# Performance work log

Hardware: AMD Instinct MI355X
Metric: run time of the kernel (lower is better)

## Reference

```python
import jax, jax.numpy as jnp
import numpy as np

B, L, LF = 4096, 200, 100
E, P, H = 64, 32, 32      # embed_dim, prompt_embed_dim, prompt_net_hidden_size
IV, UV = 100000, 50000    # item/user vocab
IFD, UFD = 128, 128       # item/user raw feature dims
PNET = E * H + H + H * P + P  # per-sample MLP param count


def _forward(item_emb, user_emb, W_if, b_if, W_uf, b_uf, Wp, bp,
             Wf1, bf1, Wf2, bf2, Wf3, item_features, user_features,
             user_id, target_item_id, history_item_id, history_len,
             item_pos_feedback, item_pos_feedback_mask,
             item_neg_feedback, item_neg_feedback_mask):
    # ---- backbone embeddings ----
    tgt = item_emb[target_item_id]              # [B,E]
    hist = item_emb[history_item_id]            # [B,L,E]
    item_feat_e = jax.nn.sigmoid(item_features @ W_if + b_if)   # [B,E]
    user_feat_e = jax.nn.sigmoid(user_features @ W_uf + b_uf)   # [B,E]
    # attention sequence pooling over history (length-masked softmax)
    valid = jnp.arange(L)[None, :] < history_len[:, None]        # [B,L]
    scores = jnp.einsum('be,ble->bl', tgt, hist) / jnp.sqrt(jnp.float32(E))
    scores = jnp.where(valid, scores, jnp.float32(-1e9))
    attn = jax.nn.softmax(scores, axis=-1)
    hist_pooled = jnp.einsum('bl,ble->be', attn, hist)           # [B,E]
    final_user_embed = user_emb[user_id] + user_feat_e + hist_pooled  # [B,E]
    final_item_embed = tgt + item_feat_e                              # [B,E]

    # ---- prompt input: masked mean over positive feedback ----
    pos_fb = item_emb[item_pos_feedback]        # [B,LF,E]
    pm = item_pos_feedback_mask.astype(jnp.float32)   # [B,LF,1]
    prompt_input = (pos_fb * pm).sum(axis=1) / pm.sum(axis=1)   # [B,E]

    # ---- hypernetwork: generate per-sample MLP weights ----
    total_prompt = jax.nn.relu(prompt_input @ Wp + bp)  # [B, P+PNET]
    prompt_embed = total_prompt[:, :P]
    pnet = total_prompt[:, P:]
    s1 = E * H
    w1 = pnet[:, :s1].reshape(-1, E, H)                 # [B,E,H]
    b1 = pnet[:, s1:s1 + H]                             # [B,H]
    w2 = pnet[:, s1 + H:s1 + H + H * P].reshape(-1, H, P)  # [B,H,P]
    b2 = pnet[:, s1 + H + H * P:]                       # [B,P]

    def prompt_mlp(u):  # u: [B,Lf,E] -> [B,Lf,P]
        h = jax.nn.relu(jnp.einsum('ble,beh->blh', u, w1) + b1[:, None, :])
        return jnp.einsum('blh,bhp->blp', h, w2) + b2[:, None, :]

    pos_pe = jnp.where(item_pos_feedback_mask, prompt_mlp(pos_fb), 0.0).sum(axis=1)  # [B,P]
    neg_fb = item_emb[item_neg_feedback]
    neg_pe = jnp.where(item_neg_feedback_mask, prompt_mlp(neg_fb), 0.0).sum(axis=1)  # [B,P]
    loss_pfpe = jax.nn.softplus(-(pos_pe - neg_pe))     # [B,P]

    # ---- fusion + dot-product scoring ----
    fusion_in = jnp.concatenate([final_item_embed, pos_pe, prompt_embed], axis=1)  # [B,E+2P]
    h = jax.nn.relu(fusion_in @ Wf1 + bf1)
    h = jax.nn.relu(h @ Wf2 + bf2)
    fused_item = h @ Wf3                                # [B,E], last layer: no bias/act
    output = jnp.sum(final_user_embed * fused_item, axis=1, keepdims=True)  # [B,1]
    return output, loss_pfpe


def setup_inputs() -> dict:
    key = jax.random.key(0)
    ks = jax.random.split(key, 20)
    g = lambda i, shape, s=0.05: jax.random.normal(ks[i], shape, jnp.float32) * s
    pm = jax.random.randint(ks[14], (B, LF, 1), 0, 2).astype(bool).at[:, 0, :].set(True)
    nm = jax.random.randint(ks[15], (B, LF, 1), 0, 2).astype(bool).at[:, 0, :].set(True)
    return {
        'item_emb': g(0, (IV, E)),
        'user_emb': g(1, (UV, E)),
        'W_if': g(2, (IFD, E)), 'b_if': jnp.zeros((E,), jnp.float32),
        'W_uf': g(3, (UFD, E)), 'b_uf': jnp.zeros((E,), jnp.float32),
        'Wp': g(4, (E, P + PNET)), 'bp': jnp.zeros((P + PNET,), jnp.float32),
        'Wf1': g(5, (E + 2 * P, 200)), 'bf1': jnp.zeros((200,), jnp.float32),
        'Wf2': g(6, (200, 80)), 'bf2': jnp.zeros((80,), jnp.float32),
        'Wf3': g(7, (80, E)),
        'item_features': jax.random.normal(ks[8], (B, IFD), jnp.float32),
        'user_features': jax.random.normal(ks[9], (B, UFD), jnp.float32),
        'user_id': jax.random.randint(ks[10], (B,), 0, UV),
        'target_item_id': jax.random.randint(ks[11], (B,), 0, IV),
        'history_item_id': jax.random.randint(ks[12], (B, L), 0, IV),
        'history_len': jax.random.randint(ks[13], (B,), 1, L + 1),
        'item_pos_feedback': jax.random.randint(ks[16], (B, LF), 0, IV),
        'item_pos_feedback_mask': pm,
        'item_neg_feedback': jax.random.randint(ks[17], (B, LF), 0, IV),
        'item_neg_feedback_mask': nm,
    }


def reference(item_emb, user_emb, W_if, b_if, W_uf, b_uf, Wp, bp,
              Wf1, bf1, Wf2, bf2, Wf3, item_features, user_features,
              user_id, target_item_id, history_item_id, history_len,
              item_pos_feedback, item_pos_feedback_mask,
              item_neg_feedback, item_neg_feedback_mask):
    return _forward(item_emb, user_emb, W_if, b_if, W_uf, b_uf, Wp, bp,
                    Wf1, bf1, Wf2, bf2, Wf3, item_features, user_features,
                    user_id, target_item_id, history_item_id, history_len,
                    item_pos_feedback, item_pos_feedback_mask,
                    item_neg_feedback, item_neg_feedback_mask)
```

## Files before the change

kernel.cpp:

```cpp
#include <hip/hip_runtime.h>
#include <hip/hip_bf16.h>
#include <hip/hip_fp16.h>
#include <math.h>

#define BN 4096
#define LH 200
#define LFB 100
#define ED 64
#define PD 32
#define HD 32
#define NP 3168
#define IV 100000

typedef unsigned int uint32;
typedef __attribute__((ext_vector_type(8))) short short8;
typedef __attribute__((ext_vector_type(8))) _Float16 half8;
typedef __attribute__((ext_vector_type(4))) float f32x4;
union BF8 { uint32 u[4]; short8 v; };
union HF8 { uint32 u[4]; half8 v; };

__device__ __forceinline__ uint32 f2bf_pack(float x, float y) {
    uint32 ux = __float_as_uint(x);
    uint32 uy = __float_as_uint(y);
    uint32 bx = (ux + 0x7fffu + ((ux >> 16) & 1u)) >> 16;
    uint32 by = (uy + 0x7fffu + ((uy >> 16) & 1u)) >> 16;
    return (by << 16) | (bx & 0xffffu);
}

__device__ __forceinline__ uint32 f2h_pack(float x, float y) {
    __half2 h = __floats2half2_rn(x, y);
    return *(reinterpret_cast<uint32*>(&h));
}

__global__ __launch_bounds__(256) void k0_cvt(
    const float* __restrict__ src, uint32* __restrict__ dst)
{
    const int i = blockIdx.x * 256 + threadIdx.x;
    const float2 v = ((const float2*)src)[i];
    dst[i] = f2bf_pack(v.x, v.y);
}

__global__ __launch_bounds__(256) void k0b_cvt_wp(
    const float* __restrict__ Wp, uint32* __restrict__ WpB)
{
    const int n = blockIdx.x * 256 + threadIdx.x;
    const int kw = blockIdx.y;
    if (n < NP) {
        const float a = Wp[(size_t)(2*kw)*NP + n];
        const float b = Wp[(size_t)(2*kw+1)*NP + n];
        WpB[(size_t)n*32 + kw] = f2bf_pack(a, b);
    }
}

__global__ __launch_bounds__(256) void k0c_cvt_wf(
    const float* __restrict__ Wf1, const float* __restrict__ Wf2,
    const float* __restrict__ Wf3, uint32* __restrict__ W1B,
    uint32* __restrict__ W2B, uint32* __restrict__ W3B)
{
    const int i = blockIdx.x * 256 + threadIdx.x;
    if (i < 13312) {
        const int n = i >> 6, kw = i & 63;
        W1B[i] = (n < 200) ? f2h_pack(Wf1[(size_t)(2*kw)*200 + n],
                                      Wf1[(size_t)(2*kw+1)*200 + n]) : 0u;
    } else if (i < 22272) {
        const int j = i - 13312, n = j / 112, kw = j % 112;
        W2B[j] = (kw < 100) ? f2h_pack(Wf2[(size_t)(2*kw)*80 + n],
                                       Wf2[(size_t)(2*kw+1)*80 + n]) : 0u;
    } else if (i < 25344) {
        const int j = i - 22272, n = j / 48, kw = j % 48;
        W3B[j] = (kw < 40) ? f2h_pack(Wf3[(size_t)(2*kw)*64 + n],
                                      Wf3[(size_t)(2*kw+1)*64 + n]) : 0u;
    }
}

#define HS 33
__global__ __launch_bounds__(256, 4) void k1_gather_attn(
    const uint32* __restrict__ IEB,
    const float* __restrict__ item_emb, const float* __restrict__ user_emb,
    const float* __restrict__ W_if, const float* __restrict__ b_if,
    const float* __restrict__ W_uf, const float* __restrict__ b_uf,
    const float* __restrict__ item_features, const float* __restrict__ user_features,
    const int* __restrict__ user_id, const int* __restrict__ target_item_id,
    const int* __restrict__ hist_id, const int* __restrict__ hist_len,
    const int* __restrict__ pos_fb, const int* __restrict__ pos_mask,
    float* __restrict__ FUE, float* __restrict__ FIE, uint32* __restrict__ PINB)
{
    const int b = blockIdx.x;
    const int t = threadIdx.x;
    const int w = t >> 6;
    const int lane = t & 63;

    __shared__ __align__(16) float tgt[64];
    __shared__ float feats[256];
    __shared__ float ufe[64];
    __shared__ float scoreS[256];
    __shared__ float wred[8];
    __shared__ float part[256];
    __shared__ float part2[256];
    __shared__ float cntw[4];
    __shared__ int   hids[200];
    __shared__ uint32 hist2[200*HS];

    const int hl = hist_len[b];
    if (t < 200) hids[t] = hist_id[(size_t)b*LH + t];
    feats[t] = (t < 128) ? item_features[(size_t)b*128 + t]
                         : user_features[(size_t)b*128 + (t-128)];
    if (t < 64) tgt[t] = item_emb[(size_t)target_item_id[b]*64 + t];
    __syncthreads();

    const int kk = lane & 31;
    const int hf = lane >> 5;
    #pragma unroll
    for (int i = 0; i < 25; i++) {
        const int l = w*50 + i*2 + hf;
        hist2[l*HS + kk] = IEB[(size_t)hids[l]*32 + kk];
    }

    {
        const int wk = lane >> 1;
        const int comp = lane & 1;
        float acc = 0.f, cnt = 0.f;
        const int l0 = w * 25;
        const int* pid = pos_fb + (size_t)b*LFB;
        const int* pmk = pos_mask + (size_t)b*LFB;
        for (int g = 0; g < 5; g++) {
            const int base = l0 + g*5;
            int m0 = pmk[base+0], m1 = pmk[base+1], m2 = pmk[base+2],
                m3 = pmk[base+3], m4 = pmk[base+4];
            int i0 = pid[base+0], i1 = pid[base+1], i2 = pid[base+2],
                i3 = pid[base+3], i4 = pid[base+4];
            uint32 w0 = IEB[(size_t)i0*32 + wk];
            uint32 w1 = IEB[(size_t)i1*32 + wk];
            uint32 w2 = IEB[(size_t)i2*32 + wk];
            uint32 w3 = IEB[(size_t)i3*32 + wk];
            uint32 w4 = IEB[(size_t)i4*32 + wk];
            float v0 = __uint_as_float(comp ? (w0 & 0xffff0000u) : (w0 << 16));
            float v1 = __uint_as_float(comp ? (w1 & 0xffff0000u) : (w1 << 16));
            float v2 = __uint_as_float(comp ? (w2 & 0xffff0000u) : (w2 << 16));
            float v3 = __uint_as_float(comp ? (w3 & 0xffff0000u) : (w3 << 16));
            float v4 = __uint_as_float(comp ? (w4 & 0xffff0000u) : (w4 << 16));
            float f0 = m0 ? 1.f : 0.f, f1 = m1 ? 1.f : 0.f, f2 = m2 ? 1.f : 0.f,
                  f3 = m3 ? 1.f : 0.f, f4 = m4 ? 1.f : 0.f;
            acc = fmaf(f0, v0, acc); acc = fmaf(f1, v1, acc);
            acc = fmaf(f2, v2, acc); acc = fmaf(f3, v3, acc);
            acc = fmaf(f4, v4, acc);
            cnt += f0 + f1 + f2 + f3 + f4;
        }
        part2[w*64 + lane] = acc;
        if (lane == 0) cntw[w] = cnt;
    }

    if (w == 0) {
        float acc = b_if[lane];
        #pragma unroll 4
        for (int k = 0; k < 128; k++) acc = fmaf(feats[k], W_if[k*64 + lane], acc);
        FIE[(size_t)b*64 + lane] = tgt[lane] + 1.f / (1.f + __expf(-acc));
    } else if (w == 1) {
        float acc = b_uf[lane];
        #pragma unroll 4
        for (int k = 0; k < 128; k++) acc = fmaf(feats[128 + k], W_uf[k*64 + lane], acc);
        ufe[lane] = 1.f / (1.f + __expf(-acc));
    }
    __syncthreads();

    float sc = -1e9f;
    if (t < 200) {
        const uint32* hrow = &hist2[t*HS];
        float acc = 0.f;
        #pragma unroll 8
        for (int k2 = 0; k2 < 32; k2++) {
            const uint32 word = hrow[k2];
            const float2 tf = ((const float2*)tgt)[k2];
            acc = fmaf(__uint_as_float(word << 16),        tf.x, acc);
            acc = fmaf(__uint_as_float(word & 0xffff0000u), tf.y, acc);
        }
        if (t < hl) sc = acc * 0.125f;
    }

    float m = sc;
    #pragma unroll
    for (int off = 32; off >= 1; off >>= 1) m = fmaxf(m, __shfl_xor(m, off, 64));
    if (lane == 0) wred[w] = m;
    __syncthreads();
    const float mx = fmaxf(fmaxf(wred[0], wred[1]), fmaxf(wred[2], wred[3]));
    const float ev = __expf(sc - mx);
    float s = ev;
    #pragma unroll
    for (int off = 32; off >= 1; off >>= 1) s += __shfl_xor(s, off, 64);
    if (lane == 0) wred[4 + w] = s;
    __syncthreads();
    const float S = wred[4] + wred[5] + wred[6] + wred[7];
    if (t < 200) scoreS[t] = ev / S;
    __syncthreads();

    {
        const int comp = lane & 1;
        const int wk = lane >> 1;
        float acc = 0.f;
        #pragma unroll 5
        for (int l = w*50; l < w*50 + 50; l++) {
            const uint32 word = hist2[l*HS + wk];
            const float hv = __uint_as_float(comp ? (word & 0xffff0000u) : (word << 16));
            acc = fmaf(scoreS[l], hv, acc);
        }
        part[w*64 + lane] = acc;
    }
    __syncthreads();

    if (t < 64) {
        const float c = cntw[0] + cntw[1] + cntw[2] + cntw[3];
        const float pooled = part[t] + part[64+t] + part[128+t] + part[192+t];
        const float pinv = (part2[t] + part2[64+t] + part2[128+t] + part2[192+t]) / c;
        FUE[(size_t)b*64 + t] = user_emb[(size_t)user_id[b]*64 + t] + ufe[t] + pooled;
        const float po = __shfl_xor(pinv, 1, 64);
        if ((t & 1) == 0) PINB[(size_t)b*32 + (t >> 1)] = f2bf_pack(pinv, po);
    }
}

__global__ __launch_bounds__(256) void k2_prompt_gemm(
    const uint32* __restrict__ PINB, const uint32* __restrict__ WpB,
    const float* __restrict__ bp, float* __restrict__ TP32,
    uint32* __restrict__ TPN)
{
    __shared__ uint32 As[64*36];
    __shared__ uint32 Bs[128*36];
    __shared__ float bps[128];
    const int t = threadIdx.x;
    const int m0 = blockIdx.y * 64;
    const int n0 = blockIdx.x * 128;

    {
        const int m = t >> 2, kw0 = (t & 3) * 8;
        const uint4 u0 = *(const uint4*)&PINB[(size_t)(m0+m)*32 + kw0];
        const uint4 u1 = *(const uint4*)&PINB[(size_t)(m0+m)*32 + kw0 + 4];
        *(uint4*)&As[m*36 + kw0]     = u0;
        *(uint4*)&As[m*36 + kw0 + 4] = u1;
    }
    {
        const int n = t >> 1, kw0 = (t & 1) * 16;
        const int gn = n0 + n;
        if (gn < NP) {
            #pragma unroll
            for (int j = 0; j < 4; j++) {
                const uint4 u = *(const uint4*)&WpB[(size_t)gn*32 + kw0 + 4*j];
                *(uint4*)&Bs[n*36 + kw0 + 4*j] = u;
            }
        } else {
            #pragma unroll
            for (int j = 0; j < 16; j++) Bs[n*36 + kw0 + j] = 0u;
        }
    }
    if (t < 128) bps[t] = (n0 + t < NP) ? bp[n0 + t] : 0.f;
    __syncthreads();

    const int w = t >> 6, lane = t & 63, ml = lane & 15, q = lane >> 4;

    BF8 a0, a1;
    { uint4 u = *(const uint4*)&As[(w*16+ml)*36 + q*4];      a0.u[0]=u.x; a0.u[1]=u.y; a0.u[2]=u.z; a0.u[3]=u.w; }
    { uint4 u = *(const uint4*)&As[(w*16+ml)*36 + 16 + q*4]; a1.u[0]=u.x; a1.u[1]=u.y; a1.u[2]=u.z; a1.u[3]=u.w; }

    f32x4 c[8];
    #pragma unroll
    for (int nb = 0; nb < 8; nb++) {
        BF8 b0, b1;
        { uint4 u = *(const uint4*)&Bs[(nb*16+ml)*36 + q*4];      b0.u[0]=u.x; b0.u[1]=u.y; b0.u[2]=u.z; b0.u[3]=u.w; }
        { uint4 u = *(const uint4*)&Bs[(nb*16+ml)*36 + 16 + q*4]; b1.u[0]=u.x; b1.u[1]=u.y; b1.u[2]=u.z; b1.u[3]=u.w; }
        f32x4 cc = {0.f, 0.f, 0.f, 0.f};
        cc = __builtin_amdgcn_mfma_f32_16x16x32_bf16(a0.v, b0.v, cc, 0, 0, 0);
        cc = __builtin_amdgcn_mfma_f32_16x16x32_bf16(a1.v, b1.v, cc, 0, 0, 0);
        c[nb] = cc;
    }

    #pragma unroll
    for (int nb = 0; nb < 8; nb++) {
        const int n = n0 + nb*16 + ml;
        const float bv = bps[nb*16 + ml];
        #pragma unroll
        for (int r = 0; r < 4; r++) {
            const int m = m0 + w*16 + q*4 + r;
            const float v = fmaxf(c[nb][r] + bv, 0.f);
            const float vp = __shfl_xor(v, 1, 64);
            if (n < 32) {
                TP32[(size_t)m*32 + n] = v;
            } else if (n < NP && (ml & 1) == 0) {
                TPN[(size_t)m*1568 + ((n - 32) >> 1)] = f2bf_pack(v, vp);
            }
        }
    }
}

__global__ __launch_bounds__(256) void k3_prompt_mlp(
    const uint32* __restrict__ IEB,
    const int* __restrict__ pos_fb, const int* __restrict__ pos_mask,
    const int* __restrict__ neg_fb, const int* __restrict__ neg_mask,
    const uint32* __restrict__ TPN,
    float* __restrict__ POS_PE, float* __restrict__ out)
{
    const int b = blockIdx.x, t = threadIdx.x;
    const int w = t >> 6, lane = t & 63;
    const int ml = lane & 15, q = lane >> 4;

    __shared__ uint32 w1b[32*36];
    __shared__ uint32 w2b[32*20];
    __shared__ float b1s[32], b2s[32];
    __shared__ float mP[208], mN[208];
    __shared__ int ids[208];
    __shared__ float Hs[4][16*36];
    __shared__ float wps[4][4][16];

    const uint32* pnw = TPN + (size_t)b*1568;
    #pragma unroll
    for (int it = 0; it < 4; it++) {
        const int i = t + 256*it;
        const int n = i >> 5, kw = i & 31;
        const uint32 wa = pnw[kw*32 + (n >> 1)];
        const uint32 wb = pnw[kw*32 + 16 + (n >> 1)];
        const uint32 h0 = (n & 1) ? (wa >> 16) : (wa & 0xffffu);
        const uint32 h1 = (n & 1) ? (wb >> 16) : (wb & 0xffffu);
        w1b[n*36 + kw] = h0 | (h1 << 16);
    }
    #pragma unroll
    for (int it = 0; it < 2; it++) {
        const int i = t + 256*it;
        const int n = i >> 4, kw = i & 15;
        const uint32 wa = pnw[1040 + kw*32 + (n >> 1)];
        const uint32 wb = pnw[1040 + kw*32 + 16 + (n >> 1)];
        const uint32 h0 = (n & 1) ? (wa >> 16) : (wa & 0xffffu);
        const uint32 h1 = (n & 1) ? (wb >> 16) : (wb & 0xffffu);
        w2b[n*20 + kw] = h0 | (h1 << 16);
    }
    if (t < 16) {
        const uint32 wa = pnw[1024 + t];
        b1s[2*t]   = __uint_as_float(wa << 16);
        b1s[2*t+1] = __uint_as_float(wa & 0xffff0000u);
        const uint32 wb = pnw[1552 + t];
        b2s[2*t]   = __uint_as_float(wb << 16);
        b2s[2*t+1] = __uint_as_float(wb & 0xffff0000u);
    }
    if (t < 208) {
        int id = 0; float p = 0.f, nn = 0.f;
        if (t < 100) {
            id = pos_fb[(size_t)b*LFB + t];
            p  = (pos_mask[(size_t)b*LFB + t] != 0) ? 1.f : 0.f;
        } else if (t < 200) {
            const int li = t - 100;
            id = neg_fb[(size_t)b*LFB + li];
            nn = (neg_mask[(size_t)b*LFB + li] != 0) ? 1.f : 0.f;
        }
        ids[t] = id; mP[t] = p; mN[t] = nn;
    }
    __syncthreads();

    BF8 bf100, bf110, bf101, bf111, bf20, bf21;
    {
        uint4 u;
        u = *(const uint4*)&w1b[ml*36 + q*4];            bf100.u[0]=u.x; bf100.u[1]=u.y; bf100.u[2]=u.z; bf100.u[3]=u.w;
        u = *(const uint4*)&w1b[ml*36 + 16 + q*4];       bf110.u[0]=u.x; bf110.u[1]=u.y; bf110.u[2]=u.z; bf110.u[3]=u.w;
        u = *(const uint4*)&w1b[(16+ml)*36 + q*4];       bf101.u[0]=u.x; bf101.u[1]=u.y; bf101.u[2]=u.z; bf101.u[3]=u.w;
        u = *(const uint4*)&w1b[(16+ml)*36 + 16 + q*4];  bf111.u[0]=u.x; bf111.u[1]=u.y; bf111.u[2]=u.z; bf111.u[3]=u.w;
        u = *(const uint4*)&w2b[ml*20 + q*4];            bf20.u[0]=u.x;  bf20.u[1]=u.y;  bf20.u[2]=u.z;  bf20.u[3]=u.w;
        u = *(const uint4*)&w2b[(16+ml)*20 + q*4];       bf21.u[0]=u.x;  bf21.u[1]=u.y;  bf21.u[2]=u.z;  bf21.u[3]=u.w;
    }

    float accP0=0.f, accP1=0.f, accN0=0.f, accN1=0.f;
    float* hsw = Hs[w];

    for (int tile = w; tile < 13; tile += 4) {
        const int g = tile*16 + ml;
        const uint32* rowp = IEB + (size_t)ids[g]*32;
        BF8 a0, a1;
        { uint4 u = *(const uint4*)(rowp + q*4);      a0.u[0]=u.x; a0.u[1]=u.y; a0.u[2]=u.z; a0.u[3]=u.w; }
        { uint4 u = *(const uint4*)(rowp + 16 + q*4); a1.u[0]=u.x; a1.u[1]=u.y; a1.u[2]=u.z; a1.u[3]=u.w; }

        f32x4 c0 = {0.f,0.f,0.f,0.f}, c1 = {0.f,0.f,0.f,0.f};
        c0 = __builtin_amdgcn_mfma_f32_16x16x32_bf16(a0.v, bf100.v, c0, 0, 0, 0);
        c0 = __builtin_amdgcn_mfma_f32_16x16x32_bf16(a1.v, bf110.v, c0, 0, 0, 0);
        c1 = __builtin_amdgcn_mfma_f32_16x16x32_bf16(a0.v, bf101.v, c1, 0, 0, 0);
        c1 = __builtin_amdgcn_mfma_f32_16x16x32_bf16(a1.v, bf111.v, c1, 0, 0, 0);

        #pragma unroll
        for (int r = 0; r < 4; r++) {
            const int row = q*4 + r;
            hsw[row*36 + ml]      = fmaxf(c0[r] + b1s[ml],      0.f);
            hsw[row*36 + 16 + ml] = fmaxf(c1[r] + b1s[16 + ml], 0.f);
        }
        asm volatile("s_waitcnt lgkmcnt(0)" ::: "memory");

        const float4 h0 = *(const float4*)&hsw[ml*36 + q*8];
        const float4 h1 = *(const float4*)&hsw[ml*36 + q*8 + 4];
        BF8 a2;
        a2.u[0] = f2bf_pack(h0.x, h0.y);
        a2.u[1] = f2bf_pack(h0.z, h0.w);
        a2.u[2] = f2bf_pack(h1.x, h1.y);
        a2.u[3] = f2bf_pack(h1.z, h1.w);

        f32x4 d0 = {0.f,0.f,0.f,0.f}, d1 = {0.f,0.f,0.f,0.f};
        d0 = __builtin_amdgcn_mfma_f32_16x16x32_bf16(a2.v, bf20.v, d0, 0, 0, 0);
        d1 = __builtin_amdgcn_mfma_f32_16x16x32_bf16(a2.v, bf21.v, d1, 0, 0, 0);

        #pragma unroll
        for (int r = 0; r < 4; r++) {
            const int g2 = tile*16 + q*4 + r;
            const float o0 = d0[r] + b2s[ml];
            const float o1 = d1[r] + b2s[16 + ml];
            accP0 = fmaf(mP[g2], o0, accP0);
            accP1 = fmaf(mP[g2], o1, accP1);
            accN0 = fmaf(mN[g2], o0, accN0);
            accN1 = fmaf(mN[g2], o1, accN1);
        }
    }

    accP0 += __shfl_xor(accP0, 16, 64); accP0 += __shfl_xor(accP0, 32, 64);
    accP1 += __shfl_xor(accP1, 16, 64); accP1 += __shfl_xor(accP1, 32, 64);
    accN0 += __shfl_xor(accN0, 16, 64); accN0 += __shfl_xor(accN0, 32, 64);
    accN1 += __shfl_xor(accN1, 16, 64); accN1 += __shfl_xor(accN1, 32, 64);
    if (lane < 16) {
        wps[w][0][lane] = accP0;
        wps[w][1][lane] = accP1;
        wps[w][2][lane] = accN0;
        wps[w][3][lane] = accN1;
    }
    __syncthreads();

    if (t < 32) {
        const int nt = t >> 4, p = t & 15;
        const float pp = wps[0][nt][p] + wps[1][nt][p] + wps[2][nt][p] + wps[3][nt][p];
        const float nn = wps[0][2+nt][p] + wps[1][2+nt][p] + wps[2][2+nt][p] + wps[3][2+nt][p];
        POS_PE[(size_t)b*32 + t] = pp;
        const float x = nn - pp;
        out[BN + (size_t)b*32 + t] = fmaxf(x, 0.f) + log1pf(__expf(-fabsf(x)));
    }
}

__global__ __launch_bounds__(256) void k4_fusion(
    const float* __restrict__ FUE, const float* __restrict__ FIE,
    const float* __restrict__ POS_PE, const float* __restrict__ TP32,
    const uint32* __restrict__ W1B, const uint32* __restrict__ W2B,
    const uint32* __restrict__ W3B,
    const float* __restrict__ bf1, const float* __restrict__ bf2,
    float* __restrict__ out)
{
    const int b0 = blockIdx.x * 16;
    const int t = threadIdx.x;
    const int w = t >> 6, lane = t & 63, ml = lane & 15, q = lane >> 4;

    __shared__ uint32 w1s[208*68];
    __shared__ uint32 w2s[80*116];
    __shared__ uint32 w3s[64*52];
    __shared__ uint32 fin[16*68];
    __shared__ uint32 h1w[16*116];
    __shared__ uint32 h2w[16*52];
    __shared__ float fuels[16*68];
    __shared__ float b1s[208], b2s[80];
    __shared__ float part4[4][16];

    for (int i = t; i < 13312; i += 256) w1s[(i >> 6)*68 + (i & 63)] = W1B[i];
    for (int i = t; i < 8960; i += 256)  w2s[(i / 112)*116 + (i % 112)] = W2B[i];
    for (int i = t; i < 3072; i += 256)  w3s[(i / 48)*52 + (i % 48)] = W3B[i];

    #pragma unroll
    for (int it = 0; it < 4; it++) {
        const int i = t + 256*it;
        const int m2 = i >> 6, kw = i & 63;
        const int row = b0 + m2;
        float a, c;
        if (kw < 32)      { const float2 v = *(const float2*)&FIE[(size_t)row*64 + 2*kw];          a = v.x; c = v.y; }
        else if (kw < 48) { const float2 v = *(const float2*)&POS_PE[(size_t)row*32 + 2*kw - 64];  a = v.x; c = v.y; }
        else              { const float2 v = *(const float2*)&TP32[(size_t)row*32 + 2*kw - 96];    a = v.x; c = v.y; }
        fin[m2*68 + kw] = f2h_pack(a, c);
        fuels[m2*68 + kw] = FUE[(size_t)row*64 + kw];
    }
    if (t < 208) b1s[t] = (t < 200) ? bf1[t] : 0.f;
    if (t < 80)  b2s[t] = bf2[t];
    if (t < 128) {
        h1w[(t >> 3)*116 + 104 + (t & 7)] = 0u;
        h2w[(t >> 3)*52 + 40 + (t & 7)] = 0u;
    }
    __syncthreads();

    HF8 a1f[4];
    #pragma unroll
    for (int s = 0; s < 4; s++) {
        const uint4 u = *(const uint4*)&fin[ml*68 + s*16 + q*4];
        a1f[s].u[0] = u.x; a1f[s].u[1] = u.y; a1f[s].u[2] = u.z; a1f[s].u[3] = u.w;
    }
    for (int nt = w; nt < 13; nt += 4) {
        const uint32* wrow = &w1s[(16*nt + ml)*68];
        f32x4 c = {0.f, 0.f, 0.f, 0.f};
        #pragma unroll
        for (int s = 0; s < 4; s++) {
            HF8 bfm;
            const uint4 u = *(const uint4*)&wrow[s*16 + q*4];
            bfm.u[0] = u.x; bfm.u[1] = u.y; bfm.u[2] = u.z; bfm.u[3] = u.w;
            c = __builtin_amdgcn_mfma_f32_16x16x32_f16(a1f[s].v, bfm.v, c, 0, 0, 0);
        }
        const float bv = b1s[16*nt + ml];
        #pragma unroll
        for (int r = 0; r < 4; r++) {
            const float v = fmaxf(c[r] + bv, 0.f);
            const float vp = __shfl_xor(v, 1, 64);
            if ((ml & 1) == 0)
                h1w[(q*4 + r)*116 + 8*nt + (ml >> 1)] = f2h_pack(v, vp);
        }
    }
    __syncthreads();

    HF8 a2f[7];
    #pragma unroll
    for (int s = 0; s < 7; s++) {
        const uint4 u = *(const uint4*)&h1w[ml*116 + s*16 + q*4];
        a2f[s].u[0] = u.x; a2f[s].u[1] = u.y; a2f[s].u[2] = u.z; a2f[s].u[3] = u.w;
    }
    for (int nt = w; nt < 5; nt += 4) {
        const uint32* wrow = &w2s[(16*nt + ml)*116];
        f32x4 c = {0.f, 0.f, 0.f, 0.f};
        #pragma unroll
        for (int s = 0; s < 7; s++) {
            HF8 bfm;
            const uint4 u = *(const uint4*)&wrow[s*16 + q*4];
            bfm.u[0] = u.x; bfm.u[1] = u.y; bfm.u[2] = u.z; bfm.u[3] = u.w;
            c = __builtin_amdgcn_mfma_f32_16x16x32_f16(a2f[s].v, bfm.v, c, 0, 0, 0);
        }
        const float bv = b2s[16*nt + ml];
        #pragma unroll
        for (int r = 0; r < 4; r++) {
            const float v = fmaxf(c[r] + bv, 0.f);
            const float vp = __shfl_xor(v, 1, 64);
            if ((ml & 1) == 0)
                h2w[(q*4 + r)*52 + 8*nt + (ml >> 1)] = f2h_pack(v, vp);
        }
    }
    __syncthreads();

    {
        const int nt = w;
        const uint32* wrow = &w3s[(16*nt + ml)*52];
        f32x4 c = {0.f, 0.f, 0.f, 0.f};
        #pragma unroll
        for (int s = 0; s < 3; s++) {
            HF8 afm, bfm;
            const uint4 ua = *(const uint4*)&h2w[ml*52 + s*16 + q*4];
            afm.u[0] = ua.x; afm.u[1] = ua.y; afm.u[2] = ua.z; afm.u[3] = ua.w;
            const uint4 ub = *(const uint4*)&wrow[s*16 + q*4];
            bfm.u[0] = ub.x; bfm.u[1] = ub.y; bfm.u[2] = ub.z; bfm.u[3] = ub.w;
            c = __builtin_amdgcn_mfma_f32_16x16x32_f16(afm.v, bfm.v, c, 0, 0, 0);
        }
        #pragma unroll
        for (int r = 0; r < 4; r++) {
            float p = c[r] * fuels[(q*4 + r)*68 + 16*nt + ml];
            p += __shfl_xor(p, 1, 64);
            p += __shfl_xor(p, 2, 64);
            p += __shfl_xor(p, 4, 64);
            p += __shfl_xor(p, 8, 64);
            if (ml == 0) part4[w][q*4 + r] = p;
        }
    }
    __syncthreads();

    if (t < 16) out[b0 + t] = part4[0][t] + part4[1][t] + part4[2][t] + part4[3][t];
}

extern "C" void kernel_launch(void* const* d_in, const int* in_sizes, int n_in,
                              void* d_out, int out_size, void* d_ws, size_t ws_size,
                              hipStream_t stream)
{
    const float* item_emb       = (const float*)d_in[0];
    const float* user_emb       = (const float*)d_in[1];
    const float* W_if           = (const float*)d_in[2];
    const float* b_if           = (const float*)d_in[3];
    const float* W_uf           = (const float*)d_in[4];
    const float* b_uf           = (const float*)d_in[5];
    const float* Wp             = (const float*)d_in[6];
    const float* bp             = (const float*)d_in[7];
    const float* Wf1            = (const float*)d_in[8];
    const float* bf1            = (const float*)d_in[9];
    const float* Wf2            = (const float*)d_in[10];
    const float* bf2            = (const float*)d_in[11];
    const float* Wf3            = (const float*)d_in[12];
    const float* item_features  = (const float*)d_in[13];
    const float* user_features  = (const float*)d_in[14];
    const int*   user_id        = (const int*)d_in[15];
    const int*   target_item_id = (const int*)d_in[16];
    const int*   history_item_id= (const int*)d_in[17];
    const int*   history_len    = (const int*)d_in[18];
    const int*   pos_fb         = (const int*)d_in[19];
    const int*   pos_mask       = (const int*)d_in[20];
    const int*   neg_fb         = (const int*)d_in[21];
    const int*   neg_mask       = (const int*)d_in[22];

    float* out = (float*)d_out;
    float* ws  = (float*)d_ws;

    uint32* IEB  = (uint32*)ws;
    uint32* WpB  = IEB + (size_t)IV*32;
    uint32* W1B  = WpB + (size_t)NP*32;
    uint32* W2B  = W1B + 13312;
    uint32* W3B  = W2B + 8960;
    uint32* PINB = W3B + 3072;
    float*  FUE  = (float*)(PINB + (size_t)BN*32);
    float*  FIE  = FUE + (size_t)BN*64;
    float*  TP32 = FIE + (size_t)BN*64;
    uint32* TPN  = (uint32*)(TP32 + (size_t)BN*32);
    float*  PPE  = (float*)(TPN + (size_t)BN*1568);

    k0_cvt<<<dim3(IV*32/256), dim3(256), 0, stream>>>(item_emb, IEB);
    k0b_cvt_wp<<<dim3(13, 32), dim3(256), 0, stream>>>(Wp, WpB);
    k0c_cvt_wf<<<dim3(99), dim3(256), 0, stream>>>(Wf1, Wf2, Wf3, W1B, W2B, W3B);

    k1_gather_attn<<<dim3(BN), dim3(256), 0, stream>>>(
        IEB, item_emb, user_emb, W_if, b_if, W_uf, b_uf,
        item_features, user_features, user_id, target_item_id,
        history_item_id, history_len, pos_fb, pos_mask,
        FUE, FIE, PINB);

    k2_prompt_gemm<<<dim3(25, 64), dim3(256), 0, stream>>>(PINB, WpB, bp, TP32, TPN);

    k3_prompt_mlp<<<dim3(BN), dim3(256), 0, stream>>>(
        IEB, pos_fb, pos_mask, neg_fb, neg_mask, TPN, PPE, out);

    k4_fusion<<<dim3(BN/16), dim3(256), 0, stream>>>(
        FUE, FIE, PPE, TP32, W1B, W2B, W3B, bf1, bf2, out);
}
```

Before: 264.5 us.

## Compact masked feedback IDs and skip history rows beyond length

The first kernel now gathers only history rows below history_len and uses ballot and prefix-count to compact the active positive-feedback ids, so the masked mean reads only active embeddings. The third kernel compacts active positive and negative feedback ids into one dense list and runs MFMA tiles only over the active count instead of all 13 tiles. The score computation and max reduction are reordered to overlap with the feedback gather. This removes wasted gathers and matrix work on masked or padded entries, at the cost of an extra barrier and ballot logic, plus load imbalance across warps when counts vary.

After: 261.9 us. About the same (-1.0%).

```diff
diff --git a/kernel.cpp b/kernel.cpp
--- a/kernel.cpp
+++ b/kernel.cpp
@@ -97,8 +97,9 @@
     __shared__ float wred[8];
     __shared__ float part[256];
     __shared__ float part2[256];
-    __shared__ float cntw[4];
     __shared__ int   hids[200];
+    __shared__ int   cpi[104];
+    __shared__ int   ptot[2];
     __shared__ uint32 hist2[200*HS];
 
     const int hl = hist_len[b];
@@ -106,49 +107,67 @@
     feats[t] = (t < 128) ? item_features[(size_t)b*128 + t]
                          : user_features[(size_t)b*128 + (t-128)];
     if (t < 64) tgt[t] = item_emb[(size_t)target_item_id[b]*64 + t];
+
+    bool myAct = false; int myPid = 0;
+    if (t < LFB) {
+        myAct = pos_mask[(size_t)b*LFB + t] != 0;
+        myPid = pos_fb[(size_t)b*LFB + t];
+    }
     __syncthreads();
 
     const int kk = lane & 31;
     const int hf = lane >> 5;
-    #pragma unroll
-    for (int i = 0; i < 25; i++) {
-        const int l = w*50 + i*2 + hf;
+    for (int l = w*2 + hf; l < hl; l += 8)
         hist2[l*HS + kk] = IEB[(size_t)hids[l]*32 + kk];
-    }
-
+
+    int pre = 0;
+    if (w < 2) {
+        const unsigned long long bal = __ballot(myAct);
+        pre = __popcll(bal & ((1ull << lane) - 1ull));
+        if (lane == 0) ptot[w] = __popcll(bal);
+    }
+    __syncthreads();
+
+    const int nP = ptot[0] + ptot[1];
+    if (w < 2 && myAct) cpi[((w == 1) ? ptot[0] : 0) + pre] = myPid;
+
+    float sc = -1e9f;
+    if (t < hl) {
+        const uint32* hrow = &hist2[t*HS];
+        float acc = 0.f;
+        #pragma unroll 8
+        for (int k2 = 0; k2 < 32; k2++) {
+            const uint32 word = hrow[k2];
+            const float2 tf = ((const float2*)tgt)[k2];
+            acc = fmaf(__uint_as_float(word << 16),         tf.x, acc);
+            acc = fmaf(__uint_as_float(word & 0xffff0000u), tf.y, acc);
+        }
+        sc = acc * 0.125f;
+    }
+    float m = sc;
+    #pragma unroll
+    for (int off = 32; off >= 1; off >>= 1) m = fmaxf(m, __shfl_xor(m, off, 64));
+    if (lane == 0) wred[w] = m;
+    __syncthreads();
+
+    const float mx = fmaxf(fmaxf(wred[0], wred[1]), fmaxf(wred[2], wred[3]));
+    const float ev = __expf(sc - mx);
+
+    const int wk = lane >> 1;
+    const int comp = lane & 1;
     {
-        const int wk = lane >> 1;
-        const int comp = lane & 1;
-        float acc = 0.f, cnt = 0.f;
-        const int l0 = w * 25;
-        const int* pid = pos_fb + (size_t)b*LFB;
-        const int* pmk = pos_mask + (size_t)b*LFB;
-        for (int g = 0; g < 5; g++) {
-            const int base = l0 + g*5;
-            int m0 = pmk[base+0], m1 = pmk[base+1], m2 = pmk[base+2],
-                m3 = pmk[base+3], m4 = pmk[base+4];
-            int i0 = pid[base+0], i1 = pid[base+1], i2 = pid[base+2],
-                i3 = pid[base+3], i4 = pid[base+4];
-            uint32 w0 = IEB[(size_t)i0*32 + wk];
-            uint32 w1 = IEB[(size_t)i1*32 + wk];
-            uint32 w2 = IEB[(size_t)i2*32 + wk];
-            uint32 w3 = IEB[(size_t)i3*32 + wk];
-            uint32 w4 = IEB[(size_t)i4*32 + wk];
-            float v0 = __uint_as_float(comp ? (w0 & 0xffff0000u) : (w0 << 16));
-            float v1 = __uint_as_float(comp ? (w1 & 0xffff0000u) : (w1 << 16));
-            float v2 = __uint_as_float(comp ? (w2 & 0xffff0000u) : (w2 << 16));
-            float v3 = __uint_as_float(comp ? (w3 & 0xffff0000u) : (w3 << 16));
-            float v4 = __uint_as_float(comp ? (w4 & 0xffff0000u) : (w4 << 16));
-            float f0 = m0 ? 1.f : 0.f, f1 = m1 ? 1.f : 0.f, f2 = m2 ? 1.f : 0.f,
-                  f3 = m3 ? 1.f : 0.f, f4 = m4 ? 1.f : 0.f;
-            acc = fmaf(f0, v0, acc); acc = fmaf(f1, v1, acc);
-            acc = fmaf(f2, v2, acc); acc = fmaf(f3, v3, acc);
-            acc = fmaf(f4, v4, acc);
-            cnt += f0 + f1 + f2 + f3 + f4;
-        }
-        part2[w*64 + lane] = acc;
-        if (lane == 0) cntw[w] = cnt;
-    }
+        float pacc = 0.f;
+        for (int i = w; i < nP; i += 4) {
+            const uint32 wd = IEB[(size_t)cpi[i]*32 + wk];
+            pacc += __uint_as_float(comp ? (wd & 0xffff0000u) : (wd << 16));
+        }
+        part2[w*64 + lane] = pacc;
+    }
+
+    float s = ev;
+    #pragma unroll
+    for (int off = 32; off >= 1; off >>= 1) s += __shfl_xor(s, off, 64);
+    if (lane == 0) wred[4 + w] = s;
 
     if (w == 0) {
         float acc = b_if[lane];
@@ -163,42 +182,13 @@
     }
     __syncthreads();
 
-    float sc = -1e9f;
-    if (t < 200) {
-        const uint32* hrow = &hist2[t*HS];
-        float acc = 0.f;
-        #pragma unroll 8
-        for (int k2 = 0; k2 < 32; k2++) {
-            const uint32 word = hrow[k2];
-            const float2 tf = ((const float2*)tgt)[k2];
-            acc = fmaf(__uint_as_float(word << 16),        tf.x, acc);
-            acc = fmaf(__uint_as_float(word & 0xffff0000u), tf.y, acc);
-        }
-        if (t < hl) sc = acc * 0.125f;
-    }
-
-    float m = sc;
-    #pragma unroll
-    for (int off = 32; off >= 1; off >>= 1) m = fmaxf(m, __shfl_xor(m, off, 64));
-    if (lane == 0) wred[w] = m;
-    __syncthreads();
-    const float mx = fmaxf(fmaxf(wred[0], wred[1]), fmaxf(wred[2], wred[3]));
-    const float ev = __expf(sc - mx);
-    float s = ev;
-    #pragma unroll
-    for (int off = 32; off >= 1; off >>= 1) s += __shfl_xor(s, off, 64);
-    if (lane == 0) wred[4 + w] = s;
-    __syncthreads();
     const float S = wred[4] + wred[5] + wred[6] + wred[7];
     if (t < 200) scoreS[t] = ev / S;
     __syncthreads();
 
     {
-        const int comp = lane & 1;
-        const int wk = lane >> 1;
         float acc = 0.f;
-        #pragma unroll 5
-        for (int l = w*50; l < w*50 + 50; l++) {
+        for (int l = w; l < hl; l += 4) {
             const uint32 word = hist2[l*HS + wk];
             const float hv = __uint_as_float(comp ? (word & 0xffff0000u) : (word << 16));
             acc = fmaf(scoreS[l], hv, acc);
@@ -208,9 +198,8 @@
     __syncthreads();
 
     if (t < 64) {
-        const float c = cntw[0] + cntw[1] + cntw[2] + cntw[3];
         const float pooled = part[t] + part[64+t] + part[128+t] + part[192+t];
-        const float pinv = (part2[t] + part2[64+t] + part2[128+t] + part2[192+t]) / c;
+        const float pinv = (part2[t] + part2[64+t] + part2[128+t] + part2[192+t]) / (float)nP;
         FUE[(size_t)b*64 + t] = user_emb[(size_t)user_id[b]*64 + t] + ufe[t] + pooled;
         const float po = __shfl_xor(pinv, 1, 64);
         if ((t & 1) == 0) PINB[(size_t)b*32 + (t >> 1)] = f2bf_pack(pinv, po);
@@ -303,10 +292,24 @@
     __shared__ uint32 w1b[32*36];
     __shared__ uint32 w2b[32*20];
     __shared__ float b1s[32], b2s[32];
-    __shared__ float mP[208], mN[208];
-    __shared__ int ids[208];
+    __shared__ float mPs[208], mNs[208];
+    __shared__ int cids[208];
+    __shared__ int tot[4];
     __shared__ float Hs[4][16*36];
     __shared__ float wps[4][4][16];
+
+    bool act = false; int id = 0;
+    if (t < LFB) {
+        act = pos_mask[(size_t)b*LFB + t] != 0;
+        id  = pos_fb[(size_t)b*LFB + t];
+    } else if (t >= 128 && t < 128 + LFB) {
+        act = neg_mask[(size_t)b*LFB + (t-128)] != 0;
+        id  = neg_fb[(size_t)b*LFB + (t-128)];
+    }
+    const unsigned long long bal = __ballot(act);
+    const int pre = __popcll(bal & ((1ull << lane) - 1ull));
+    if (lane == 0) tot[w] = __popcll(bal);
+    if (t < 208) cids[t] = 0;
 
     const uint32* pnw = TPN + (size_t)b*1568;
     #pragma unroll
@@ -337,19 +340,23 @@
         b2s[2*t]   = __uint_as_float(wb << 16);
         b2s[2*t+1] = __uint_as_float(wb & 0xffff0000u);
     }
+    __syncthreads();
+
+    const int nP = tot[0] + tot[1];
+    const int nN = tot[2] + tot[3];
+    const int R  = nP + nN;
+    const int T  = (R + 15) >> 4;
+    {
+        int base = 0;
+        if (w == 1) base = tot[0];
+        else if (w == 2) base = nP;
+        else if (w == 3) base = nP + tot[2];
+        if (act) cids[base + pre] = id;
+    }
     if (t < 208) {
-        int id = 0; float p = 0.f, nn = 0.f;
-        if (t < 100) {
-            id = pos_fb[(size_t)b*LFB + t];
-            p  = (pos_mask[(size_t)b*LFB + t] != 0) ? 1.f : 0.f;
-        } else if (t < 200) {
-            const int li = t - 100;
-            id = neg_fb[(size_t)b*LFB + li];
-            nn = (neg_mask[(size_t)b*LFB + li] != 0) ? 1.f : 0.f;
-        }
-        ids[t] = id; mP[t] = p; mN[t] = nn;
-    }
-    __syncthreads();
+        mPs[t] = (t < nP) ? 1.f : 0.f;
+        mNs[t] = (t >= nP && t < R) ? 1.f : 0.f;
+    }
 
     BF8 bf100, bf110, bf101, bf111, bf20, bf21;
     {
@@ -361,13 +368,14 @@
         u = *(const uint4*)&w2b[ml*20 + q*4];            bf20.u[0]=u.x;  bf20.u[1]=u.y;  bf20.u[2]=u.z;  bf20.u[3]=u.w;
         u = *(const uint4*)&w2b[(16+ml)*20 + q*4];       bf21.u[0]=u.x;  bf21.u[1]=u.y;  bf21.u[2]=u.z;  bf21.u[3]=u.w;
     }
+    __syncthreads();
 
     float accP0=0.f, accP1=0.f, accN0=0.f, accN1=0.f;
     float* hsw = Hs[w];
 
-    for (int tile = w; tile < 13; tile += 4) {
+    for (int tile = w; tile < T; tile += 4) {
         const int g = tile*16 + ml;
-        const uint32* rowp = IEB + (size_t)ids[g]*32;
+        const uint32* rowp = IEB + (size_t)cids[g]*32;
         BF8 a0, a1;
         { uint4 u = *(const uint4*)(rowp + q*4);      a0.u[0]=u.x; a0.u[1]=u.y; a0.u[2]=u.z; a0.u[3]=u.w; }
         { uint4 u = *(const uint4*)(rowp + 16 + q*4); a1.u[0]=u.x; a1.u[1]=u.y; a1.u[2]=u.z; a1.u[3]=u.w; }
@@ -403,10 +411,10 @@
             const int g2 = tile*16 + q*4 + r;
             const float o0 = d0[r] + b2s[ml];
             const float o1 = d1[r] + b2s[16 + ml];
-            accP0 = fmaf(mP[g2], o0, accP0);
-            accP1 = fmaf(mP[g2], o1, accP1);
-            accN0 = fmaf(mN[g2], o0, accN0);
-            accN1 = fmaf(mN[g2], o1, accN1);
+            accP0 = fmaf(mPs[g2], o0, accP0);
+            accP1 = fmaf(mPs[g2], o1, accP1);
+            accN0 = fmaf(mNs[g2], o0, accN0);
+            accN1 = fmaf(mNs[g2], o1, accN1);
         }
     }
 
```
